# Performance work log

Measured on AMD Instinct MI355X. Metric: run time of the kernel, lower is better.

## Reference

```python
import jax, jax.numpy as jnp
import numpy as np


def setup_inputs() -> dict:
    key = jax.random.key(0)
    k_u, k_wl, k_b, k_c = jax.random.split(key, 4)
    B_, T, D, N = 4, 4096, 1024, 256
    u = jax.random.normal(k_u, (B_, T, D), dtype=jnp.float32)
    # torch init: W_lambda.weight zeros, bias 2.0; B, C xavier_uniform gain=0.5.
    # Use small random weights for W_lambda too so the path is exercised.
    Wl = jax.random.normal(k_wl, (N, D), dtype=jnp.float32) * 0.02
    bl = jnp.full((N,), 2.0, dtype=jnp.float32)
    xav_b = 0.5 * np.sqrt(6.0 / (D + N))
    Wb = jax.random.uniform(k_b, (N, D), dtype=jnp.float32, minval=-xav_b, maxval=xav_b)
    xav_c = 0.5 * np.sqrt(6.0 / (N + D))
    Wc = jax.random.uniform(k_c, (D, N), dtype=jnp.float32, minval=-xav_c, maxval=xav_c)
    Dp = jnp.zeros((D,), dtype=jnp.float32)
    return {"u": u, "Wl": Wl, "bl": bl, "Wb": Wb, "Wc": Wc, "Dp": Dp}


def reference(u, Wl, bl, Wb, Wc, Dp):
    # u: (B, T, D). Precompute per-step gates and inputs with batched GEMMs,
    # then run the diagonal linear recurrence with lax.scan over time.
    lam = jax.nn.sigmoid(jnp.einsum('btd,nd->btn', u, Wl) + bl)  # (B, T, N)
    Bu = jnp.einsum('btd,nd->btn', u, Wb)                         # (B, T, N)

    def step(h, inp):
        lam_t, bu_t = inp            # each (B, N)
        h = lam_t * h + bu_t
        return h, h

    h0 = jnp.zeros((u.shape[0], Wl.shape[0]), dtype=u.dtype)
    # scan over time: move T to leading axis
    _, H = jax.lax.scan(step, h0, (jnp.swapaxes(lam, 0, 1), jnp.swapaxes(Bu, 0, 1)))
    H = jnp.swapaxes(H, 0, 1)        # (B, T, N)
    y = jnp.einsum('btn,dn->btd', H, Wc) + u * Dp
    return y
```

## Files before the change

### kernel.cpp

```cpp
#include <hip/hip_runtime.h>


typedef __bf16 bf16_t;
typedef __attribute__((ext_vector_type(8))) __bf16 bf16x8;
typedef __attribute__((ext_vector_type(4))) __bf16 bf16x4;
typedef __attribute__((ext_vector_type(4))) float f32x4;

#define B_  4
#define T_  4096
#define D_  1024
#define N_  256
#define BT  (B_ * T_)
#define NCHUNK 32
#define CHLEN  (T_ / NCHUNK)

#define GLOAD_LDS16(g, l) __builtin_amdgcn_global_load_lds(              \
    (__attribute__((address_space(1))) void*)(g),                        \
    (__attribute__((address_space(3))) void*)(l), 16, 0, 0)

__global__ void cvt_f32_bf16(const float* __restrict__ in,
                             bf16_t* __restrict__ out, int n4) {
  int i = blockIdx.x * 256 + threadIdx.x;
  if (i >= n4) return;
  float4 v = ((const float4*)in)[i];
  bf16x4 o = {(__bf16)v.x, (__bf16)v.y, (__bf16)v.z, (__bf16)v.w};
  ((bf16x4*)out)[i] = o;
}

__global__ void cvt_wcomb(const float* __restrict__ Wl,
                          const float* __restrict__ Wb,
                          bf16_t* __restrict__ out) {
  int i = blockIdx.x * 256 + threadIdx.x;
  int e = i * 4;
  int j = e >> 10;
  int d = e & 1023;
  const float* src = (j < 256) ? (Wl + (size_t)j * D_ + d)
                               : (Wb + (size_t)(j - 256) * D_ + d);
  float4 v = *(const float4*)src;
  bf16x4 o = {(__bf16)v.x, (__bf16)v.y, (__bf16)v.z, (__bf16)v.w};
  ((bf16x4*)out)[i] = o;
}

__global__ __launch_bounds__(256)
void gemm1_kernel(const float* __restrict__ A, const bf16_t* __restrict__ Bm,
                  float* __restrict__ C, int M, int N, int K,
                  const float* __restrict__ bl) {
  __shared__ bf16_t lA[128 * 64];
  __shared__ bf16_t lB[128 * 64];
  const int wid  = threadIdx.x >> 6;
  const int lane = threadIdx.x & 63;
  const int brow = blockIdx.x;
  const int bcol = blockIdx.y;
  const int r16 = lane & 15;
  const int kq  = lane >> 4;
  const int wr = wid >> 1, wc = wid & 1;

  f32x4 acc[4][4] = {};

  const int ar = lane >> 4;
  const int ac = (lane & 15) * 4;
  const float* gA = A + (size_t)(brow * 128 + wid * 32 + ar) * K + ac;
  bf16_t* lAw = &lA[(wid * 32 + ar) * 64 + ac];

  const int srow = wid * 8 + (lane >> 3);
  const int scol = (lane & 7) * 8;
  const bf16_t* gB = Bm + (size_t)(bcol * 128 + srow) * K + scol;
  bf16_t* lBd = &lB[(wid * 8) * 64];

  for (int k0 = 0; k0 < K; k0 += 64) {
    float4 va[8];
#pragma unroll
    for (int i = 0; i < 8; ++i)
      va[i] = *(const float4*)(gA + (size_t)(i * 4) * K + k0);
#pragma unroll
    for (int i = 0; i < 4; ++i)
      GLOAD_LDS16(gB + (size_t)(i * 32) * K + k0, lBd + i * 32 * 64);
#pragma unroll
    for (int i = 0; i < 8; ++i) {
      bf16x4 o = {(__bf16)va[i].x, (__bf16)va[i].y,
                  (__bf16)va[i].z, (__bf16)va[i].w};
      *(bf16x4*)(lAw + i * 4 * 64) = o;
    }
    __syncthreads();
#pragma unroll
    for (int kk = 0; kk < 2; ++kk) {
      bf16x8 af[4], bfr[4];
#pragma unroll
      for (int m = 0; m < 4; ++m)
        af[m] = *(const bf16x8*)&lA[(wr * 64 + m * 16 + r16) * 64 + kk * 32 + kq * 8];
#pragma unroll
      for (int n = 0; n < 4; ++n)
        bfr[n] = *(const bf16x8*)&lB[(wc * 64 + n * 16 + r16) * 64 + kk * 32 + kq * 8];
#pragma unroll
      for (int m = 0; m < 4; ++m)
#pragma unroll
        for (int n = 0; n < 4; ++n)
          acc[m][n] = __builtin_amdgcn_mfma_f32_16x16x32_bf16(af[m], bfr[n], acc[m][n], 0, 0, 0);
    }
    __syncthreads();
  }

#pragma unroll
  for (int m = 0; m < 4; ++m) {
#pragma unroll
    for (int n = 0; n < 4; ++n) {
      int row0 = brow * 128 + wr * 64 + m * 16 + kq * 4;
      int col  = bcol * 128 + wc * 64 + n * 16 + r16;
#pragma unroll
      for (int j = 0; j < 4; ++j) {
        float v = acc[m][n][j];
        int row = row0 + j;
        if (col < 256) v = 1.0f / (1.0f + __expf(-(v + bl[col])));
        C[(size_t)row * N + col] = v;
      }
    }
  }
}

__global__ __launch_bounds__(256)
void gemm2_kernel(const bf16_t* __restrict__ A, const bf16_t* __restrict__ Bm,
                  float* __restrict__ C, int M, int N, int K,
                  const float* __restrict__ u, const float* __restrict__ Dp) {
  __shared__ bf16_t lA[128 * 64];
  __shared__ bf16_t lB[128 * 64];
  const int wid  = threadIdx.x >> 6;
  const int lane = threadIdx.x & 63;
  const int brow = blockIdx.x;
  const int bcol = blockIdx.y;
  const int r16 = lane & 15;
  const int kq  = lane >> 4;
  const int wr = wid >> 1, wc = wid & 1;

  f32x4 acc[4][4] = {};

  const int srow = wid * 8 + (lane >> 3);
  const int scol = (lane & 7) * 8;
  const bf16_t* gA = A + (size_t)(brow * 128 + srow) * K + scol;
  const bf16_t* gB = Bm + (size_t)(bcol * 128 + srow) * K + scol;
  bf16_t* lAd = &lA[(wid * 8) * 64];
  bf16_t* lBd = &lB[(wid * 8) * 64];

  for (int k0 = 0; k0 < K; k0 += 64) {
#pragma unroll
    for (int i = 0; i < 4; ++i) {
      GLOAD_LDS16(gA + (size_t)(i * 32) * K + k0, lAd + i * 32 * 64);
      GLOAD_LDS16(gB + (size_t)(i * 32) * K + k0, lBd + i * 32 * 64);
    }
    __syncthreads();
#pragma unroll
    for (int kk = 0; kk < 2; ++kk) {
      bf16x8 af[4], bfr[4];
#pragma unroll
      for (int m = 0; m < 4; ++m)
        af[m] = *(const bf16x8*)&lA[(wr * 64 + m * 16 + r16) * 64 + kk * 32 + kq * 8];
#pragma unroll
      for (int n = 0; n < 4; ++n)
        bfr[n] = *(const bf16x8*)&lB[(wc * 64 + n * 16 + r16) * 64 + kk * 32 + kq * 8];
#pragma unroll
      for (int m = 0; m < 4; ++m)
#pragma unroll
        for (int n = 0; n < 4; ++n)
          acc[m][n] = __builtin_amdgcn_mfma_f32_16x16x32_bf16(af[m], bfr[n], acc[m][n], 0, 0, 0);
    }
    __syncthreads();
  }

#pragma unroll
  for (int m = 0; m < 4; ++m) {
#pragma unroll
    for (int n = 0; n < 4; ++n) {
      int row0 = brow * 128 + wr * 64 + m * 16 + kq * 4;
      int col  = bcol * 128 + wc * 64 + n * 16 + r16;
#pragma unroll
      for (int j = 0; j < 4; ++j) {
        int row = row0 + j;
        float v = acc[m][n][j] + Dp[col] * u[(size_t)row * N + col];
        C[(size_t)row * N + col] = v;
      }
    }
  }
}

__global__ void scan_phase1(const float* __restrict__ Z,
                            float* __restrict__ wsA, float* __restrict__ wsB) {
  int tid = blockIdx.x * 256 + threadIdx.x;
  int n = tid & 255;
  int chunk = (tid >> 8) & 31;
  int b = tid >> 13;
  const float* zl = Z + ((size_t)(b * T_ + chunk * CHLEN)) * 512 + n;
  float A = 1.f, h = 0.f;
#pragma unroll 4
  for (int t = 0; t < CHLEN; ++t) {
    float lam = zl[0];
    float bu  = zl[256];
    A *= lam;
    h = fmaf(lam, h, bu);
    zl += 512;
  }
  wsA[tid] = A;
  wsB[tid] = h;
}

__global__ void scan_phase2(const float* __restrict__ wsA,
                            const float* __restrict__ wsB,
                            float* __restrict__ carry) {
  int tid = blockIdx.x * 256 + threadIdx.x;
  int n = tid & 255;
  int b = tid >> 8;
  float h = 0.f;
#pragma unroll
  for (int c = 0; c < NCHUNK; ++c) {
    int idx = (b * NCHUNK + c) * 256 + n;
    carry[idx] = h;
    h = fmaf(wsA[idx], h, wsB[idx]);
  }
}

__global__ void scan_phase3(const float* __restrict__ Z,
                            const float* __restrict__ carry,
                            bf16_t* __restrict__ H) {
  int tid = blockIdx.x * 256 + threadIdx.x;
  int n = tid & 255;
  int chunk = (tid >> 8) & 31;
  int b = tid >> 13;
  const float* zl = Z + ((size_t)(b * T_ + chunk * CHLEN)) * 512 + n;
  bf16_t* ho = H + ((size_t)(b * T_ + chunk * CHLEN)) * 256 + n;
  float h = carry[tid];
#pragma unroll 4
  for (int t = 0; t < CHLEN; ++t) {
    float lam = zl[0];
    float bu  = zl[256];
    h = fmaf(lam, h, bu);
    *ho = (__bf16)h;
    zl += 512;
    ho += 256;
  }
}

extern "C" void kernel_launch(void* const* d_in, const int* in_sizes, int n_in,
                              void* d_out, int out_size, void* d_ws, size_t ws_size,
                              hipStream_t stream) {
  const float* u  = (const float*)d_in[0];
  const float* Wl = (const float*)d_in[1];
  const float* bl = (const float*)d_in[2];
  const float* Wb = (const float*)d_in[3];
  const float* Wc = (const float*)d_in[4];
  const float* Dp = (const float*)d_in[5];
  float* y = (float*)d_out;

  char* ws = (char*)d_ws;
  float*  Z     = (float*)(ws + 0);
  bf16_t* H     = (bf16_t*)(ws + 33554432);
  bf16_t* Wcomb = (bf16_t*)(ws + 41943040);
  bf16_t* Wc_bf = (bf16_t*)(ws + 42991616);
  float*  wsA   = (float*)(ws + 43515904);
  float*  wsB   = (float*)(ws + 43646976);
  float*  carry = (float*)(ws + 43778048);

  cvt_wcomb<<<(512 * D_ / 4) / 256, 256, 0, stream>>>(Wl, Wb, Wcomb);
  cvt_f32_bf16<<<(D_ * N_ / 4) / 256, 256, 0, stream>>>(Wc, Wc_bf, D_ * N_ / 4);

  dim3 g1(BT / 128, 512 / 128);
  gemm1_kernel<<<g1, 256, 0, stream>>>(u, Wcomb, Z, BT, 512, D_, bl);

  scan_phase1<<<(B_ * NCHUNK * N_) / 256, 256, 0, stream>>>(Z, wsA, wsB);
  scan_phase2<<<(B_ * N_) / 256, 256, 0, stream>>>(wsA, wsB, carry);
  scan_phase3<<<(B_ * NCHUNK * N_) / 256, 256, 0, stream>>>(Z, carry, H);

  dim3 g2(BT / 128, D_ / 128);
  gemm2_kernel<<<g2, 256, 0, stream>>>(H, Wc_bf, y, BT, D_, N_, u, Dp);
}
```

Measured before the change: 221.1 us.

## Double-buffer LDS in both GEMMs, remap gemm1 blocks, and double scan chunks

Both GEMM kernels now use two LDS buffers, so the global loads for the next K-tile are issued before the MFMA work on the current tile, and each iteration needs one barrier instead of two. gemm1 moves to a 1D grid of 512 blocks with a remapped block index that spreads consecutive blocks across row tiles, likely to improve cache or XCD locality. The scan uses 64 chunks instead of 32, which doubles the parallelism of phases 1 and 3, and their unroll factor is raised. The costs are double the LDS per block, which may lower occupancy, and a longer serial pass in scan phase 2.

```diff
diff --git a/kernel.cpp b/kernel.cpp
--- a/kernel.cpp
+++ b/kernel.cpp
@@ -11,7 +11,7 @@
 #define D_  1024
 #define N_  256
 #define BT  (B_ * T_)
-#define NCHUNK 32
+#define NCHUNK 64
 #define CHLEN  (T_ / NCHUNK)
 
 #define GLOAD_LDS16(g, l) __builtin_amdgcn_global_load_lds(              \
@@ -41,12 +41,113 @@
   ((bf16x4*)out)[i] = o;
 }
 
+__device__ __forceinline__ void mfma_tile(const bf16_t* bufA, const bf16_t* bufB,
+                                          int wr, int wc, int r16, int kq,
+                                          f32x4 (&acc)[4][4]) {
+#pragma unroll
+  for (int kk = 0; kk < 2; ++kk) {
+    bf16x8 af[4], bfr[4];
+#pragma unroll
+    for (int m = 0; m < 4; ++m)
+      af[m] = *(const bf16x8*)&bufA[(wr * 64 + m * 16 + r16) * 64 + kk * 32 + kq * 8];
+#pragma unroll
+    for (int n = 0; n < 4; ++n)
+      bfr[n] = *(const bf16x8*)&bufB[(wc * 64 + n * 16 + r16) * 64 + kk * 32 + kq * 8];
+#pragma unroll
+    for (int m = 0; m < 4; ++m)
+#pragma unroll
+      for (int n = 0; n < 4; ++n)
+        acc[m][n] = __builtin_amdgcn_mfma_f32_16x16x32_bf16(af[m], bfr[n], acc[m][n], 0, 0, 0);
+  }
+}
+
 __global__ __launch_bounds__(256)
 void gemm1_kernel(const float* __restrict__ A, const bf16_t* __restrict__ Bm,
-                  float* __restrict__ C, int M, int N, int K,
-                  const float* __restrict__ bl) {
-  __shared__ bf16_t lA[128 * 64];
-  __shared__ bf16_t lB[128 * 64];
+                  float* __restrict__ C, const float* __restrict__ bl) {
+  __shared__ bf16_t lA[2][128 * 64];
+  __shared__ bf16_t lB[2][128 * 64];
+  const int wid  = threadIdx.x >> 6;
+  const int lane = threadIdx.x & 63;
+  const int work = (blockIdx.x & 7) * 64 + (blockIdx.x >> 3);
+  const int brow = work >> 2;
+  const int bcol = work & 3;
+  const int r16 = lane & 15;
+  const int kq  = lane >> 4;
+  const int wr = wid >> 1, wc = wid & 1;
+
+  f32x4 acc[4][4] = {};
+
+  const int ar = lane >> 4;
+  const int ac = (lane & 15) * 4;
+  const float* gA = A + (size_t)(brow * 128 + wid * 32 + ar) * D_ + ac;
+  bf16_t* lAw[2] = {&lA[0][(wid * 32 + ar) * 64 + ac],
+                    &lA[1][(wid * 32 + ar) * 64 + ac]};
+
+  const bf16_t* gB = Bm + (size_t)(bcol * 128 + wid * 8 + (lane >> 3)) * D_ + (lane & 7) * 8;
+
+  {
+    float4 va[8];
+#pragma unroll
+    for (int i = 0; i < 8; ++i)
+      va[i] = *(const float4*)(gA + (size_t)(i * 4) * D_);
+#pragma unroll
+    for (int i = 0; i < 4; ++i)
+      GLOAD_LDS16(gB + (size_t)(i * 32) * D_, &lB[0][(wid * 8 + i * 32) * 64]);
+#pragma unroll
+    for (int i = 0; i < 8; ++i) {
+      bf16x4 o = {(__bf16)va[i].x, (__bf16)va[i].y,
+                  (__bf16)va[i].z, (__bf16)va[i].w};
+      *(bf16x4*)(lAw[0] + i * 4 * 64) = o;
+    }
+    __syncthreads();
+  }
+
+  int cur = 0;
+#pragma unroll 1
+  for (int k0 = 0; k0 < D_ - 64; k0 += 64) {
+    float4 va[8];
+#pragma unroll
+    for (int i = 0; i < 8; ++i)
+      va[i] = *(const float4*)(gA + (size_t)(i * 4) * D_ + k0 + 64);
+#pragma unroll
+    for (int i = 0; i < 4; ++i)
+      GLOAD_LDS16(gB + (size_t)(i * 32) * D_ + k0 + 64,
+                  &lB[cur ^ 1][(wid * 8 + i * 32) * 64]);
+    mfma_tile(lA[cur], lB[cur], wr, wc, r16, kq, acc);
+#pragma unroll
+    for (int i = 0; i < 8; ++i) {
+      bf16x4 o = {(__bf16)va[i].x, (__bf16)va[i].y,
+                  (__bf16)va[i].z, (__bf16)va[i].w};
+      *(bf16x4*)(lAw[cur ^ 1] + i * 4 * 64) = o;
+    }
+    __syncthreads();
+    cur ^= 1;
+  }
+  mfma_tile(lA[cur], lB[cur], wr, wc, r16, kq, acc);
+
+#pragma unroll
+  for (int m = 0; m < 4; ++m) {
+#pragma unroll
+    for (int n = 0; n < 4; ++n) {
+      int row0 = brow * 128 + wr * 64 + m * 16 + kq * 4;
+      int col  = bcol * 128 + wc * 64 + n * 16 + r16;
+#pragma unroll
+      for (int j = 0; j < 4; ++j) {
+        float v = acc[m][n][j];
+        int row = row0 + j;
+        if (col < 256) v = 1.0f / (1.0f + __expf(-(v + bl[col])));
+        C[(size_t)row * 512 + col] = v;
+      }
+    }
+  }
+}
+
+__global__ __launch_bounds__(256)
+void gemm2_kernel(const bf16_t* __restrict__ A, const bf16_t* __restrict__ Bm,
+                  float* __restrict__ C,
+                  const float* __restrict__ u, const float* __restrict__ Dp) {
+  __shared__ bf16_t lA[2][128 * 64];
+  __shared__ bf16_t lB[2][128 * 64];
   const int wid  = threadIdx.x >> 6;
   const int lane = threadIdx.x & 63;
   const int brow = blockIdx.x;
@@ -57,48 +158,32 @@
 
   f32x4 acc[4][4] = {};
 
-  const int ar = lane >> 4;
-  const int ac = (lane & 15) * 4;
-  const float* gA = A + (size_t)(brow * 128 + wid * 32 + ar) * K + ac;
-  bf16_t* lAw = &lA[(wid * 32 + ar) * 64 + ac];
-
-  const int srow = wid * 8 + (lane >> 3);
-  const int scol = (lane & 7) * 8;
-  const bf16_t* gB = Bm + (size_t)(bcol * 128 + srow) * K + scol;
-  bf16_t* lBd = &lB[(wid * 8) * 64];
-
-  for (int k0 = 0; k0 < K; k0 += 64) {
-    float4 va[8];
-#pragma unroll
-    for (int i = 0; i < 8; ++i)
-      va[i] = *(const float4*)(gA + (size_t)(i * 4) * K + k0);
-#pragma unroll
-    for (int i = 0; i < 4; ++i)
-      GLOAD_LDS16(gB + (size_t)(i * 32) * K + k0, lBd + i * 32 * 64);
-#pragma unroll
-    for (int i = 0; i < 8; ++i) {
-      bf16x4 o = {(__bf16)va[i].x, (__bf16)va[i].y,
-                  (__bf16)va[i].z, (__bf16)va[i].w};
-      *(bf16x4*)(lAw + i * 4 * 64) = o;
-    }
-    __syncthreads();
-#pragma unroll
-    for (int kk = 0; kk < 2; ++kk) {
-      bf16x8 af[4], bfr[4];
-#pragma unroll
-      for (int m = 0; m < 4; ++m)
-        af[m] = *(const bf16x8*)&lA[(wr * 64 + m * 16 + r16) * 64 + kk * 32 + kq * 8];
-#pragma unroll
-      for (int n = 0; n < 4; ++n)
-        bfr[n] = *(const bf16x8*)&lB[(wc * 64 + n * 16 + r16) * 64 + kk * 32 + kq * 8];
-#pragma unroll
-      for (int m = 0; m < 4; ++m)
-#pragma unroll
-        for (int n = 0; n < 4; ++n)
-          acc[m][n] = __builtin_amdgcn_mfma_f32_16x16x32_bf16(af[m], bfr[n], acc[m][n], 0, 0, 0);
-    }
-    __syncthreads();
-  }
+  const bf16_t* gA = A + (size_t)(brow * 128 + wid * 8 + (lane >> 3)) * N_ + (lane & 7) * 8;
+  const bf16_t* gB = Bm + (size_t)(bcol * 128 + wid * 8 + (lane >> 3)) * N_ + (lane & 7) * 8;
+
+  {
+#pragma unroll
+    for (int i = 0; i < 4; ++i) {
+      GLOAD_LDS16(gA + (size_t)(i * 32) * N_, &lA[0][(wid * 8 + i * 32) * 64]);
+      GLOAD_LDS16(gB + (size_t)(i * 32) * N_, &lB[0][(wid * 8 + i * 32) * 64]);
+    }
+    __syncthreads();
+  }
+  int cur = 0;
+#pragma unroll 1
+  for (int k0 = 0; k0 < N_ - 64; k0 += 64) {
+#pragma unroll
+    for (int i = 0; i < 4; ++i) {
+      GLOAD_LDS16(gA + (size_t)(i * 32) * N_ + k0 + 64,
+                  &lA[cur ^ 1][(wid * 8 + i * 32) * 64]);
+      GLOAD_LDS16(gB + (size_t)(i * 32) * N_ + k0 + 64,
+                  &lB[cur ^ 1][(wid * 8 + i * 32) * 64]);
+    }
+    mfma_tile(lA[cur], lB[cur], wr, wc, r16, kq, acc);
+    __syncthreads();
+    cur ^= 1;
+  }
+  mfma_tile(lA[cur], lB[cur], wr, wc, r16, kq, acc);
 
 #pragma unroll
   for (int m = 0; m < 4; ++m) {
@@ -108,74 +193,9 @@
       int col  = bcol * 128 + wc * 64 + n * 16 + r16;
 #pragma unroll
       for (int j = 0; j < 4; ++j) {
-        float v = acc[m][n][j];
         int row = row0 + j;
-        if (col < 256) v = 1.0f / (1.0f + __expf(-(v + bl[col])));
-        C[(size_t)row * N + col] = v;
-      }
-    }
-  }
-}
-
-__global__ __launch_bounds__(256)
-void gemm2_kernel(const bf16_t* __restrict__ A, const bf16_t* __restrict__ Bm,
-                  float* __restrict__ C, int M, int N, int K,
-                  const float* __restrict__ u, const float* __restrict__ Dp) {
-  __shared__ bf16_t lA[128 * 64];
-  __shared__ bf16_t lB[128 * 64];
-  const int wid  = threadIdx.x >> 6;
-  const int lane = threadIdx.x & 63;
-  const int brow = blockIdx.x;
-  const int bcol = blockIdx.y;
-  const int r16 = lane & 15;
-  const int kq  = lane >> 4;
-  const int wr = wid >> 1, wc = wid & 1;
-
-  f32x4 acc[4][4] = {};
-
-  const int srow = wid * 8 + (lane >> 3);
-  const int scol = (lane & 7) * 8;
-  const bf16_t* gA = A + (size_t)(brow * 128 + srow) * K + scol;
-  const bf16_t* gB = Bm + (size_t)(bcol * 128 + srow) * K + scol;
-  bf16_t* lAd = &lA[(wid * 8) * 64];
-  bf16_t* lBd = &lB[(wid * 8) * 64];
-
-  for (int k0 = 0; k0 < K; k0 += 64) {
-#pragma unroll
-    for (int i = 0; i < 4; ++i) {
-      GLOAD_LDS16(gA + (size_t)(i * 32) * K + k0, lAd + i * 32 * 64);
-      GLOAD_LDS16(gB + (size_t)(i * 32) * K + k0, lBd + i * 32 * 64);
-    }
-    __syncthreads();
-#pragma unroll
-    for (int kk = 0; kk < 2; ++kk) {
-      bf16x8 af[4], bfr[4];
-#pragma unroll
-      for (int m = 0; m < 4; ++m)
-        af[m] = *(const bf16x8*)&lA[(wr * 64 + m * 16 + r16) * 64 + kk * 32 + kq * 8];
-#pragma unroll
-      for (int n = 0; n < 4; ++n)
-        bfr[n] = *(const bf16x8*)&lB[(wc * 64 + n * 16 + r16) * 64 + kk * 32 + kq * 8];
-#pragma unroll
-      for (int m = 0; m < 4; ++m)
-#pragma unroll
-        for (int n = 0; n < 4; ++n)
-          acc[m][n] = __builtin_amdgcn_mfma_f32_16x16x32_bf16(af[m], bfr[n], acc[m][n], 0, 0, 0);
-    }
-    __syncthreads();
-  }
-
-#pragma unroll
-  for (int m = 0; m < 4; ++m) {
-#pragma unroll
-    for (int n = 0; n < 4; ++n) {
-      int row0 = brow * 128 + wr * 64 + m * 16 + kq * 4;
-      int col  = bcol * 128 + wc * 64 + n * 16 + r16;
-#pragma unroll
-      for (int j = 0; j < 4; ++j) {
-        int row = row0 + j;
-        float v = acc[m][n][j] + Dp[col] * u[(size_t)row * N + col];
-        C[(size_t)row * N + col] = v;
+        float v = acc[m][n][j] + Dp[col] * u[(size_t)row * D_ + col];
+        C[(size_t)row * D_ + col] = v;
       }
     }
   }
@@ -185,11 +205,11 @@
                             float* __restrict__ wsA, float* __restrict__ wsB) {
   int tid = blockIdx.x * 256 + threadIdx.x;
   int n = tid & 255;
-  int chunk = (tid >> 8) & 31;
-  int b = tid >> 13;
+  int chunk = (tid >> 8) & (NCHUNK - 1);
+  int b = tid >> 14;
   const float* zl = Z + ((size_t)(b * T_ + chunk * CHLEN)) * 512 + n;
   float A = 1.f, h = 0.f;
-#pragma unroll 4
+#pragma unroll 8
   for (int t = 0; t < CHLEN; ++t) {
     float lam = zl[0];
     float bu  = zl[256];
@@ -221,12 +241,12 @@
                             bf16_t* __restrict__ H) {
   int tid = blockIdx.x * 256 + threadIdx.x;
   int n = tid & 255;
-  int chunk = (tid >> 8) & 31;
-  int b = tid >> 13;
+  int chunk = (tid >> 8) & (NCHUNK - 1);
+  int b = tid >> 14;
   const float* zl = Z + ((size_t)(b * T_ + chunk * CHLEN)) * 512 + n;
   bf16_t* ho = H + ((size_t)(b * T_ + chunk * CHLEN)) * 256 + n;
   float h = carry[tid];
-#pragma unroll 4
+#pragma unroll 8
   for (int t = 0; t < CHLEN; ++t) {
     float lam = zl[0];
     float bu  = zl[256];
@@ -254,19 +274,18 @@
   bf16_t* Wcomb = (bf16_t*)(ws + 41943040);
   bf16_t* Wc_bf = (bf16_t*)(ws + 42991616);
   float*  wsA   = (float*)(ws + 43515904);
-  float*  wsB   = (float*)(ws + 43646976);
-  float*  carry = (float*)(ws + 43778048);
+  float*  wsB   = (float*)(ws + 43778048);
+  float*  carry = (float*)(ws + 44040192);
 
   cvt_wcomb<<<(512 * D_ / 4) / 256, 256, 0, stream>>>(Wl, Wb, Wcomb);
   cvt_f32_bf16<<<(D_ * N_ / 4) / 256, 256, 0, stream>>>(Wc, Wc_bf, D_ * N_ / 4);
 
-  dim3 g1(BT / 128, 512 / 128);
-  gemm1_kernel<<<g1, 256, 0, stream>>>(u, Wcomb, Z, BT, 512, D_, bl);
+  gemm1_kernel<<<512, 256, 0, stream>>>(u, Wcomb, Z, bl);
 
   scan_phase1<<<(B_ * NCHUNK * N_) / 256, 256, 0, stream>>>(Z, wsA, wsB);
   scan_phase2<<<(B_ * N_) / 256, 256, 0, stream>>>(wsA, wsB, carry);
   scan_phase3<<<(B_ * NCHUNK * N_) / 256, 256, 0, stream>>>(Z, carry, H);
 
   dim3 g2(BT / 128, D_ / 128);
-  gemm2_kernel<<<g2, 256, 0, stream>>>(H, Wc_bf, y, BT, D_, N_, u, Dp);
-}
+  gemm2_kernel<<<g2, 256, 0, stream>>>(H, Wc_bf, y, u, Dp);
+}
```

Result: faster. 210.8 us (-4.7%).
